# Kernel optimization log

Measured on AMD Instinct MI355X. Metric: run time of the kernel, lower is better.

The kernel has to match this reference:

```python
import jax, jax.numpy as jnp
import numpy as np


def dense_image_warp(image, flow):
    """Port of tfa.image.dense_image_warp.
    out[b,y,x,c] = bilinear(image[b], y - flow[b,y,x,0], x - flow[b,y,x,1]).
    Query coords are clamped like tfa.image.interpolate_bilinear:
    floor clipped to [0, size-2], alpha clipped to [0, 1].
    """
    B, H, W, C = image.shape
    gy = jnp.arange(H, dtype=flow.dtype)[None, :, None]  # [1,H,1]
    gx = jnp.arange(W, dtype=flow.dtype)[None, None, :]  # [1,1,W]
    qy = gy - flow[..., 0]  # [B,H,W]
    qx = gx - flow[..., 1]

    fy = jnp.clip(jnp.floor(qy), 0.0, H - 2)
    fx = jnp.clip(jnp.floor(qx), 0.0, W - 2)
    ay = jnp.clip(qy - fy, 0.0, 1.0)[..., None]  # [B,H,W,1]
    ax = jnp.clip(qx - fx, 0.0, 1.0)[..., None]
    iy = fy.astype(jnp.int32)
    ix = fx.astype(jnp.int32)

    bidx = jnp.arange(B, dtype=jnp.int32)[:, None, None]  # [B,1,1]
    tl = image[bidx, iy, ix]          # [B,H,W,C]
    tr = image[bidx, iy, ix + 1]
    bl = image[bidx, iy + 1, ix]
    br = image[bidx, iy + 1, ix + 1]

    top = tl + ax * (tr - tl)
    bot = bl + ax * (br - bl)
    return top + ay * (bot - top)


def reference(frames_0, f_t0, v_t0, frames_1, f_t1, v_t1, t_indeces):
    g_i0_ft0 = dense_image_warp(frames_0, f_t0)
    g_i1_ft1 = dense_image_warp(frames_1, f_t1)
    w0 = (1.0 - t_indeces) * v_t0
    w1 = t_indeces * v_t1
    z = w0 + w1 + 1e-12
    frame_pred = (w0 * g_i0_ft0 + w1 * g_i1_ft1) / z
    return frame_pred


def setup_inputs() -> dict:
    key = jax.random.key(0)
    ks = jax.random.split(key, 7)
    B, H, W, C = 16, 512, 512, 3
    return {
        "frames_0": jax.random.uniform(ks[0], (B, H, W, C), jnp.float32),
        "f_t0": jax.random.normal(ks[1], (B, H, W, 2), jnp.float32) * 4.0,
        "v_t0": jax.random.uniform(ks[2], (B, H, W, 1), jnp.float32),
        "frames_1": jax.random.uniform(ks[3], (B, H, W, C), jnp.float32),
        "f_t1": jax.random.normal(ks[4], (B, H, W, 2), jnp.float32) * 4.0,
        "v_t1": jax.random.uniform(ks[5], (B, H, W, 1), jnp.float32),
        "t_indeces": jax.random.uniform(ks[6], (B, 1, 1, 1), jnp.float32),
    }
```

## Files before the change

### kernel.cpp

```cpp
#include <hip/hip_runtime.h>

#define BDIM 16
#define HDIM 512
#define WDIM 512
#define CDIM 3

struct __attribute__((aligned(4))) pf4 { float x, y, z, w; };
struct __attribute__((aligned(4))) pf2 { float x, y; };

struct Taps {
    pf4 a0; pf2 b0;
    pf4 a1; pf2 b1;
    float ax, ay;
};

__device__ __forceinline__ Taps bilinear_load(
    const float* __restrict__ img, float qy, float qx)
{
    float fy = fminf(fmaxf(floorf(qy), 0.0f), (float)(HDIM - 2));
    float fx = fminf(fmaxf(floorf(qx), 0.0f), (float)(WDIM - 2));
    Taps tp;
    tp.ay = fminf(fmaxf(qy - fy, 0.0f), 1.0f);
    tp.ax = fminf(fmaxf(qx - fx, 0.0f), 1.0f);
    int iy = (int)fy;
    int ix = (int)fx;
    const float* r0 = img + ((size_t)iy * WDIM + ix) * CDIM;
    const float* r1 = r0 + WDIM * CDIM;
    tp.a0 = *reinterpret_cast<const pf4*>(r0);
    tp.b0 = *reinterpret_cast<const pf2*>(r0 + 4);
    tp.a1 = *reinterpret_cast<const pf4*>(r1);
    tp.b1 = *reinterpret_cast<const pf2*>(r1 + 4);
    return tp;
}

__device__ __forceinline__ void bilinear_eval(const Taps& t, float g[3])
{
    float tl[3] = {t.a0.x, t.a0.y, t.a0.z};
    float tr[3] = {t.a0.w, t.b0.x, t.b0.y};
    float bl[3] = {t.a1.x, t.a1.y, t.a1.z};
    float br[3] = {t.a1.w, t.b1.x, t.b1.y};
#pragma unroll
    for (int c = 0; c < CDIM; ++c) {
        float top = tl[c] + t.ax * (tr[c] - tl[c]);
        float bot = bl[c] + t.ax * (br[c] - bl[c]);
        g[c] = top + t.ay * (bot - top);
    }
}

__global__ __launch_bounds__(256) void warp_interp_kernel(
    const float* __restrict__ frames0,
    const float* __restrict__ flow0,
    const float* __restrict__ vis0,
    const float* __restrict__ frames1,
    const float* __restrict__ flow1,
    const float* __restrict__ vis1,
    const float* __restrict__ tind,
    float* __restrict__ out)
{
    const int bid = blockIdx.x;
    const int swz = (bid & 7) * 1024 + (bid >> 3);
    const int idx = swz * 256 + threadIdx.x;
    const int STRIDE = 8192 * 256;

    const size_t pA = (size_t)idx;
    const size_t pB = pA + STRIDE;

    const int xA = (int)(pA & (WDIM - 1));
    const int yA = (int)((pA >> 9) & (HDIM - 1));
    const int bA = (int)(pA >> 18);
    const int xB = (int)(pB & (WDIM - 1));
    const int yB = (int)((pB >> 9) & (HDIM - 1));
    const int bB = (int)(pB >> 18);

    float2 f0A = *reinterpret_cast<const float2*>(flow0 + 2 * pA);
    float2 f1A = *reinterpret_cast<const float2*>(flow1 + 2 * pA);
    float2 f0B = *reinterpret_cast<const float2*>(flow0 + 2 * pB);
    float2 f1B = *reinterpret_cast<const float2*>(flow1 + 2 * pB);
    float v0A = vis0[pA], v1A = vis1[pA];
    float v0B = vis0[pB], v1B = vis1[pB];
    float tA = tind[bA], tB = tind[bB];

    const float* img0A = frames0 + (size_t)bA * HDIM * WDIM * CDIM;
    const float* img1A = frames1 + (size_t)bA * HDIM * WDIM * CDIM;
    const float* img0B = frames0 + (size_t)bB * HDIM * WDIM * CDIM;
    const float* img1B = frames1 + (size_t)bB * HDIM * WDIM * CDIM;

    Taps t0A = bilinear_load(img0A, (float)yA - f0A.x, (float)xA - f0A.y);
    Taps t1A = bilinear_load(img1A, (float)yA - f1A.x, (float)xA - f1A.y);
    Taps t0B = bilinear_load(img0B, (float)yB - f0B.x, (float)xB - f0B.y);
    Taps t1B = bilinear_load(img1B, (float)yB - f1B.x, (float)xB - f1B.y);

    __builtin_amdgcn_sched_barrier(0);

    float w0A = (1.0f - tA) * v0A, w1A = tA * v1A;
    float invA = __builtin_amdgcn_rcpf(w0A + w1A + 1e-12f);
    float w0B = (1.0f - tB) * v0B, w1B = tB * v1B;
    float invB = __builtin_amdgcn_rcpf(w0B + w1B + 1e-12f);

    float g0[3], g1[3];
    bilinear_eval(t0A, g0);
    bilinear_eval(t1A, g1);
    float* opA = out + 3 * pA;
    opA[0] = (w0A * g0[0] + w1A * g1[0]) * invA;
    opA[1] = (w0A * g0[1] + w1A * g1[1]) * invA;
    opA[2] = (w0A * g0[2] + w1A * g1[2]) * invA;

    bilinear_eval(t0B, g0);
    bilinear_eval(t1B, g1);
    float* opB = out + 3 * pB;
    opB[0] = (w0B * g0[0] + w1B * g1[0]) * invB;
    opB[1] = (w0B * g0[1] + w1B * g1[1]) * invB;
    opB[2] = (w0B * g0[2] + w1B * g1[2]) * invB;
}

extern "C" void kernel_launch(void* const* d_in, const int* in_sizes, int n_in,
                              void* d_out, int out_size, void* d_ws, size_t ws_size,
                              hipStream_t stream) {
    const float* frames0 = (const float*)d_in[0];
    const float* flow0   = (const float*)d_in[1];
    const float* vis0    = (const float*)d_in[2];
    const float* frames1 = (const float*)d_in[3];
    const float* flow1   = (const float*)d_in[4];
    const float* vis1    = (const float*)d_in[5];
    const float* tind    = (const float*)d_in[6];
    float* out = (float*)d_out;

    const int block = 256;
    const int grid = 8192;

    warp_interp_kernel<<<grid, block, 0, stream>>>(
        frames0, flow0, vis0, frames1, flow1, vis1, tind, out);
}
```

Before: 76.28 us.

## Process two adjacent pixels per thread with vectorized loads and nontemporal stores

Each block now covers one image row, and each thread handles two horizontally adjacent pixels instead of two pixels a full grid-stride apart. Flow and visibility are read with 16-byte and 8-byte vector loads, and the six output floats are written as three 8-byte nontemporal stores. The aim is fewer, wider memory instructions, better gather locality because neighbouring pixels share source taps, and output stores that bypass cache. Per-lane access is now 16B/8B strided, and the nontemporal stores may interact with write combining in ways that are hard to predict.

```diff
diff --git a/kernel.cpp b/kernel.cpp
--- a/kernel.cpp
+++ b/kernel.cpp
@@ -4,6 +4,9 @@
 #define HDIM 512
 #define WDIM 512
 #define CDIM 3
+
+typedef float f32x2 __attribute__((ext_vector_type(2)));
+typedef float f32x4 __attribute__((ext_vector_type(4)));
 
 struct __attribute__((aligned(4))) pf4 { float x, y, z, w; };
 struct __attribute__((aligned(4))) pf2 { float x, y; };
@@ -58,59 +61,53 @@
     float* __restrict__ out)
 {
     const int bid = blockIdx.x;
-    const int swz = (bid & 7) * 1024 + (bid >> 3);
-    const int idx = swz * 256 + threadIdx.x;
-    const int STRIDE = 8192 * 256;
+    const int row = (bid & 7) * 1024 + (bid >> 3);
+    const int y   = row & (HDIM - 1);
+    const int b   = row >> 9;
+    const int x0  = (int)threadIdx.x * 2;
+    const int x1  = x0 + 1;
+    const size_t P = (size_t)row * WDIM + (size_t)x0;
 
-    const size_t pA = (size_t)idx;
-    const size_t pB = pA + STRIDE;
+    f32x4 f0 = *reinterpret_cast<const f32x4*>(flow0 + 2 * P);
+    f32x4 f1 = *reinterpret_cast<const f32x4*>(flow1 + 2 * P);
+    f32x2 v0 = *reinterpret_cast<const f32x2*>(vis0 + P);
+    f32x2 v1 = *reinterpret_cast<const f32x2*>(vis1 + P);
+    const float t = tind[b];
 
-    const int xA = (int)(pA & (WDIM - 1));
-    const int yA = (int)((pA >> 9) & (HDIM - 1));
-    const int bA = (int)(pA >> 18);
-    const int xB = (int)(pB & (WDIM - 1));
-    const int yB = (int)((pB >> 9) & (HDIM - 1));
-    const int bB = (int)(pB >> 18);
+    const float* img0 = frames0 + (size_t)b * (HDIM * WDIM * CDIM);
+    const float* img1 = frames1 + (size_t)b * (HDIM * WDIM * CDIM);
 
-    float2 f0A = *reinterpret_cast<const float2*>(flow0 + 2 * pA);
-    float2 f1A = *reinterpret_cast<const float2*>(flow1 + 2 * pA);
-    float2 f0B = *reinterpret_cast<const float2*>(flow0 + 2 * pB);
-    float2 f1B = *reinterpret_cast<const float2*>(flow1 + 2 * pB);
-    float v0A = vis0[pA], v1A = vis1[pA];
-    float v0B = vis0[pB], v1B = vis1[pB];
-    float tA = tind[bA], tB = tind[bB];
-
-    const float* img0A = frames0 + (size_t)bA * HDIM * WDIM * CDIM;
-    const float* img1A = frames1 + (size_t)bA * HDIM * WDIM * CDIM;
-    const float* img0B = frames0 + (size_t)bB * HDIM * WDIM * CDIM;
-    const float* img1B = frames1 + (size_t)bB * HDIM * WDIM * CDIM;
-
-    Taps t0A = bilinear_load(img0A, (float)yA - f0A.x, (float)xA - f0A.y);
-    Taps t1A = bilinear_load(img1A, (float)yA - f1A.x, (float)xA - f1A.y);
-    Taps t0B = bilinear_load(img0B, (float)yB - f0B.x, (float)xB - f0B.y);
-    Taps t1B = bilinear_load(img1B, (float)yB - f1B.x, (float)xB - f1B.y);
+    Taps t0A = bilinear_load(img0, (float)y - f0.x, (float)x0 - f0.y);
+    Taps t1A = bilinear_load(img1, (float)y - f1.x, (float)x0 - f1.y);
+    Taps t0B = bilinear_load(img0, (float)y - f0.z, (float)x1 - f0.w);
+    Taps t1B = bilinear_load(img1, (float)y - f1.z, (float)x1 - f1.w);
 
     __builtin_amdgcn_sched_barrier(0);
 
-    float w0A = (1.0f - tA) * v0A, w1A = tA * v1A;
+    float w0A = (1.0f - t) * v0.x, w1A = t * v1.x;
     float invA = __builtin_amdgcn_rcpf(w0A + w1A + 1e-12f);
-    float w0B = (1.0f - tB) * v0B, w1B = tB * v1B;
+    float w0B = (1.0f - t) * v0.y, w1B = t * v1.y;
     float invB = __builtin_amdgcn_rcpf(w0B + w1B + 1e-12f);
 
-    float g0[3], g1[3];
+    float g0[3], g1[3], o[6];
     bilinear_eval(t0A, g0);
     bilinear_eval(t1A, g1);
-    float* opA = out + 3 * pA;
-    opA[0] = (w0A * g0[0] + w1A * g1[0]) * invA;
-    opA[1] = (w0A * g0[1] + w1A * g1[1]) * invA;
-    opA[2] = (w0A * g0[2] + w1A * g1[2]) * invA;
-
+    o[0] = (w0A * g0[0] + w1A * g1[0]) * invA;
+    o[1] = (w0A * g0[1] + w1A * g1[1]) * invA;
+    o[2] = (w0A * g0[2] + w1A * g1[2]) * invA;
     bilinear_eval(t0B, g0);
     bilinear_eval(t1B, g1);
-    float* opB = out + 3 * pB;
-    opB[0] = (w0B * g0[0] + w1B * g1[0]) * invB;
-    opB[1] = (w0B * g0[1] + w1B * g1[1]) * invB;
-    opB[2] = (w0B * g0[2] + w1B * g1[2]) * invB;
+    o[3] = (w0B * g0[0] + w1B * g1[0]) * invB;
+    o[4] = (w0B * g0[1] + w1B * g1[1]) * invB;
+    o[5] = (w0B * g0[2] + w1B * g1[2]) * invB;
+
+    float* op = out + 3 * P;
+    f32x2 s0; s0.x = o[0]; s0.y = o[1];
+    f32x2 s1; s1.x = o[2]; s1.y = o[3];
+    f32x2 s2; s2.x = o[4]; s2.y = o[5];
+    __builtin_nontemporal_store(s0, reinterpret_cast<f32x2*>(op));
+    __builtin_nontemporal_store(s1, reinterpret_cast<f32x2*>(op + 2));
+    __builtin_nontemporal_store(s2, reinterpret_cast<f32x2*>(op + 4));
 }
 
 extern "C" void kernel_launch(void* const* d_in, const int* in_sizes, int n_in,
```

Result: slower. 86.13 us (+12.9%).
